# Kernel tuning notes

Measured on AMD Instinct MI355X. Metric: run time of the kernel, lower is better.

## Reference

```python
import jax, jax.numpy as jnp
import numpy as np

SPARSITY = 0.1
B, N, K = 256, 65536, 64

def setup_inputs() -> dict:
    key = jax.random.key(0)
    kx, kc = jax.random.split(key)
    x = jax.random.normal(kx, (B, N), dtype=jnp.float32)
    cluster_assignments = jax.random.randint(kc, (N,), 0, K, dtype=jnp.int32)
    cluster_weights = jnp.ones((K,), dtype=jnp.float32)
    return {"x": x, "cluster_weights": cluster_weights, "cluster_assignments": cluster_assignments}

def reference(x, cluster_weights, cluster_assignments):
    b, n = x.shape
    k = cluster_weights.shape[0]
    # cluster activation prob (context=None path): softmax(weights), same for all batch rows
    p = jax.nn.softmax(cluster_weights) * SPARSITY                      # [K]
    ku, kv = jax.random.split(jax.random.key(42))
    u = jax.random.uniform(ku, (b, n))   # drives the random permutation per (batch, cluster)
    v = jax.random.uniform(kv, (b, n))   # drives the binomial count (sum of Bernoullis)
    # Binomial(len(cluster_i), p_i) == sum of per-neuron Bernoulli(p_i) over the cluster
    bern = (v < p[cluster_assignments][None, :]).astype(jnp.int32)      # [B, N]
    counts = jax.vmap(lambda row: jax.ops.segment_sum(row, cluster_assignments, num_segments=k))(bern)  # [B, K]
    counts = jnp.maximum(counts, 1)                                     # max(1, binomial sample)
    # within-cluster uniform-random ranking: sort by (cluster, u); rank = pos - cluster_start
    sizes = jnp.bincount(cluster_assignments, length=k)                 # [K]
    starts = jnp.cumsum(sizes) - sizes                                  # exclusive cumsum [K]
    cluster_sorted = jnp.sort(cluster_assignments)                      # [N], batch-independent
    pos_in_cluster = jnp.arange(n) - starts[cluster_sorted]             # [N]
    keys = cluster_assignments.astype(jnp.float32)[None, :] + u * 0.999  # cluster-major composite key
    order = jnp.argsort(keys, axis=1)                                   # [B, N]
    mask_sorted = (pos_in_cluster[None, :] < counts[:, cluster_sorted]).astype(x.dtype)  # [B, N]
    mask = jnp.zeros_like(x).at[jnp.arange(b)[:, None], order].set(mask_sorted)
    return x * mask
```

## Files before the change

### kernel.cpp

```cpp
#include <hip/hip_runtime.h>
#include <stdint.h>

#define NROWS 256
#define NCOLS 65536
#define KCL   64
#define TMAX  20
#define NBLK  128
#define CHUNK (NCOLS / NBLK)
#define ZBLK  2048

__device__ __forceinline__ void tf2x32(uint32_t k0, uint32_t k1,
                                       uint32_t x0, uint32_t x1,
                                       uint32_t& o0, uint32_t& o1) {
  const uint32_t ks2 = k0 ^ k1 ^ 0x1BD11BDAu;
  x0 += k0; x1 += k1;
#define TFR(r) { x0 += x1; x1 = (x1 << (r)) | (x1 >> (32 - (r))); x1 ^= x0; }
  TFR(13) TFR(15) TFR(26) TFR(6)
  x0 += k1; x1 += ks2 + 1u;
  TFR(17) TFR(29) TFR(16) TFR(24)
  x0 += ks2; x1 += k0 + 2u;
  TFR(13) TFR(15) TFR(26) TFR(6)
  x0 += k0; x1 += k1 + 3u;
  TFR(17) TFR(29) TFR(16) TFR(24)
  x0 += k1; x1 += ks2 + 4u;
  TFR(13) TFR(15) TFR(26) TFR(6)
  x0 += ks2; x1 += k0 + 5u;
#undef TFR
  o0 = x0; o1 = x1;
}

__device__ __forceinline__ uint32_t jax_bits(uint32_t k0, uint32_t k1, uint32_t f) {
  uint32_t o0, o1;
  tf2x32(k0, k1, 0u, f, o0, o1);
  return o0 ^ o1;
}

__device__ __forceinline__ float bits_to_u01(uint32_t bits) {
  return __uint_as_float((bits >> 9) | 0x3f800000u) - 1.0f;
}

__device__ __forceinline__ float key_from_ubits(uint32_t ubits, float kf) {
  return __fadd_rn(kf, __fmul_rn(bits_to_u01(ubits), 0.999f));
}

__device__ __forceinline__ int wave_sum_i(int v) {
#pragma unroll
  for (int m = 1; m < 64; m <<= 1) v += __shfl_xor(v, m, 64);
  return v;
}
__device__ __forceinline__ uint32_t wave_min_u(uint32_t v) {
#pragma unroll
  for (int m = 1; m < 64; m <<= 1) {
    const uint32_t o = (uint32_t)__shfl_xor((int)v, m, 64);
    v = (o < v) ? o : v;
  }
  return v;
}
__device__ __forceinline__ int wave_min_i(int v) {
#pragma unroll
  for (int m = 1; m < 64; m <<= 1) {
    const int o = __shfl_xor(v, m, 64);
    v = (o < v) ? o : v;
  }
  return v;
}

__global__ __launch_bounds__(256)
void k_zerohist(float4* __restrict__ outv, const int* __restrict__ a,
                int* __restrict__ blockhist) {
  const int gtid = blockIdx.x * 256 + threadIdx.x;
  const float4 z = make_float4(0.f, 0.f, 0.f, 0.f);
#pragma unroll
  for (int i = 0; i < 8; ++i)
    outv[gtid + i * (ZBLK * 256)] = z;
  if (blockIdx.x < NBLK) {
    __shared__ int h[KCL];
    if (threadIdx.x < KCL) h[threadIdx.x] = 0;
    __syncthreads();
    const int base = blockIdx.x * CHUNK;
#pragma unroll
    for (int i = base + threadIdx.x; i < base + CHUNK; i += 256)
      atomicAdd(&h[a[i]], 1);
    __syncthreads();
    if (threadIdx.x < KCL) blockhist[blockIdx.x * KCL + threadIdx.x] = h[threadIdx.x];
  }
}

__global__ void k_prefix_setup(int* __restrict__ blockhist, int* __restrict__ sizes,
                               int* __restrict__ starts,
                               const float* __restrict__ w, uint32_t* __restrict__ hdr,
                               uint32_t* __restrict__ vthresh) {
  const int k = threadIdx.x;
  int acc = 0;
#pragma unroll 8
  for (int blk = 0; blk < NBLK; ++blk) {
    const int t = blockhist[blk * KCL + k];
    blockhist[blk * KCL + k] = acc;
    acc += t;
  }
  sizes[k] = acc;
  int scan = acc;
#pragma unroll
  for (int d = 1; d < 64; d <<= 1) {
    const int o = __shfl_up(scan, d, 64);
    if (k >= d) scan += o;
  }
  starts[k] = scan - acc;
  const float wk = w[k];
  float m = wk;
#pragma unroll
  for (int d = 1; d < 64; d <<= 1) m = fmaxf(m, __shfl_xor(m, d, 64));
  const float e = expf(wk - m);
  float s = e;
#pragma unroll
  for (int d = 1; d < 64; d <<= 1) s += __shfl_xor(s, d, 64);
  const float pk = (e / s) * 0.1f;
  vthresh[k] = (uint32_t)ceilf(pk * 8388608.0f);
  if (k == 0) {
    uint32_t o0, o1;
    tf2x32(0u, 42u, 0u, 0u, o0, o1); hdr[0] = o0; hdr[1] = o1;
    tf2x32(0u, 42u, 0u, 1u, o0, o1); hdr[2] = o0; hdr[3] = o1;
  }
}

__global__ __launch_bounds__(256)
void k_scatter(const int* __restrict__ a, const int* __restrict__ blockhist,
               const int* __restrict__ starts, int* __restrict__ idx_sorted) {
  __shared__ int cur[KCL];
  const int tid = threadIdx.x;
  if (tid < KCL) cur[tid] = starts[tid] + blockhist[blockIdx.x * KCL + tid];
  __syncthreads();
  const int base = blockIdx.x * CHUNK;
#pragma unroll
  for (int i = base + tid; i < base + CHUNK; i += 256) {
    const int k = a[i];
    const int slot = atomicAdd(&cur[k], 1);
    idx_sorted[slot] = i;
  }
}

__global__ __launch_bounds__(256)
void k_select(const float* __restrict__ x,
              const int* __restrict__ idx_sorted,
              const int* __restrict__ sizes,
              const int* __restrict__ starts,
              const uint32_t* __restrict__ hdr,
              const uint32_t* __restrict__ vthresh,
              float* __restrict__ out) {
  __shared__ uint32_t kbs[TMAX][256];
  const int tid = threadIdx.x;
  const int lane = tid & 63;
  const int pair = (blockIdx.x << 2) + (tid >> 6);
  const int b = pair & (NROWS - 1);
  const int k = pair >> 8;

  int sz = sizes[k];
  const int st = starts[k];
  if (sz <= 0) return;
  if (sz > TMAX * 64) sz = TMAX * 64;

  const uint32_t ku0 = hdr[0], ku1 = hdr[1], kv0 = hdr[2], kv1 = hdr[3];
  const uint32_t vt = vthresh[k];
  const float kf = (float)k;
  const uint32_t bbase = (uint32_t)(b << 16);

  int nv_next = (lane < sz) ? idx_sorted[st + lane] : 0;
  uint32_t curmin = 0xFFFFFFFFu;
  int cnt = 0;
#pragma unroll 4
  for (int t = 0; t < TMAX; ++t) {
    const int nv = nv_next;
    const int jn = lane + ((t + 1) << 6);
    nv_next = (jn < sz) ? idx_sorted[st + jn] : 0;
    const int j = lane + (t << 6);
    uint32_t kbv = 0xFFFFFFFFu;
    if (j < sz) {
      const uint32_t f = bbase + (uint32_t)nv;
      const uint32_t ubv = jax_bits(ku0, ku1, f);
      const uint32_t vbv = jax_bits(kv0, kv1, f);
      cnt += ((vbv >> 9) < vt) ? 1 : 0;
      kbv = __float_as_uint(key_from_ubits(ubv, kf));
    }
    kbs[t][tid] = kbv;
    curmin = (kbv < curmin) ? kbv : curmin;
  }
  int C = wave_sum_i(cnt);
  if (C < 1) C = 1;

  uint32_t consumed = 0;
  uint32_t Tkey;
  for (int e = 0;; ++e) {
    const uint32_t wmn = wave_min_u(curmin);
    if (e == C - 1) { Tkey = wmn; break; }
    const unsigned long long bal = __ballot(curmin == wmn);
    const int src = (int)__ffsll((long long)bal) - 1;
    if (lane == src) {
      int ct = -1;
      for (int t = 0; t < TMAX; ++t)
        if (ct < 0 && !((consumed >> t) & 1u) && kbs[t][tid] == wmn) ct = t;
      consumed |= (1u << ct);
      uint32_t nm = 0xFFFFFFFFu;
      for (int t = 0; t < TMAX; ++t) {
        const uint32_t v = ((consumed >> t) & 1u) ? 0xFFFFFFFFu : kbs[t][tid];
        nm = (v < nm) ? v : nm;
      }
      curmin = nm;
    }
  }

  int packed = 0;
#pragma unroll 4
  for (int t = 0; t < TMAX; ++t) {
    const uint32_t v = kbs[t][tid];
    packed += (v < Tkey) ? (1 << 16) : 0;
    packed += (v == Tkey) ? 1 : 0;
  }
  const int sred = wave_sum_i(packed);
  const int nbelow = sred >> 16;
  const int tieCnt = sred & 0xFFFF;
  const int r = C - nbelow;

  int cutN = 0x7FFFFFFF;
  if (r < tieCnt) {
    uint32_t cons2 = 0;
    for (int e = 0; e < r; ++e) {
      int mnN = 0x7FFFFFFF, mnT = 0;
      for (int t = 0; t < TMAX; ++t) {
        if (kbs[t][tid] == Tkey && !((cons2 >> t) & 1u)) {
          const int n = idx_sorted[st + lane + (t << 6)];
          if (n < mnN) { mnN = n; mnT = t; }
        }
      }
      const int w = wave_min_i(mnN);
      cutN = w;
      const unsigned long long bal = __ballot(mnN == w);
      const int src = (int)__ffsll((long long)bal) - 1;
      if (lane == src) cons2 |= (1u << mnT);
    }
  }

  const size_t rowoff = (size_t)b * NCOLS;
#pragma unroll 4
  for (int t = 0; t < TMAX; ++t) {
    const uint32_t v = kbs[t][tid];
    bool sel = (v < Tkey);
    if (!sel && v == Tkey) {
      if (r >= tieCnt) {
        sel = true;
      } else {
        const int n = idx_sorted[st + lane + (t << 6)];
        sel = (n <= cutN);
      }
    }
    if (sel) {
      const int n = idx_sorted[st + lane + (t << 6)];
      const size_t off = rowoff + (uint32_t)n;
      out[off] = x[off];
    }
  }
}

extern "C" void kernel_launch(void* const* d_in, const int* in_sizes, int n_in,
                              void* d_out, int out_size, void* d_ws, size_t ws_size,
                              hipStream_t stream) {
  const float* x = (const float*)d_in[0];
  const float* w = (const float*)d_in[1];
  const int* assign = (const int*)d_in[2];
  float* out = (float*)d_out;
  uint32_t* ws = (uint32_t*)d_ws;

  uint32_t* hdr       = ws;
  uint32_t* vthresh   = ws + 4;
  int*      sizes     = (int*)(ws + 68);
  int*      starts    = (int*)(ws + 132);
  int*      blockhist = (int*)(ws + 196);
  int*      idxs      = (int*)(ws + 196 + NBLK * KCL);

  k_zerohist<<<ZBLK, 256, 0, stream>>>((float4*)out, assign, blockhist);
  k_prefix_setup<<<1, 64, 0, stream>>>(blockhist, sizes, starts, w, hdr, vthresh);
  k_scatter<<<NBLK, 256, 0, stream>>>(assign, blockhist, starts, idxs);
  k_select<<<(NROWS * KCL) / 4, 256, 0, stream>>>(x, idxs, sizes, starts, hdr, vthresh, out);
  (void)n_in; (void)in_sizes; (void)ws_size;
}
```

Measured before the change: 111.2 us.

## Bound per-wave loops by cluster size, use DPP reductions, regroup blocks by cluster

The select kernel's loops now run only over the cluster's actual number of 64-wide tiles (tcap) instead of always TMAX, which skips Threefry hashing and LDS scans on padding slots. Wave reductions switch from shfl_xor loops to DPP and ds_swizzle steps, and the rotate uses a builtin. Block-to-(batch, cluster) mapping changes so each block's four waves share one cluster k, making sizes and idx_sorted reads uniform per block. A side effect is that the main loop loses its software-prefetch of indices.

```diff
diff --git a/kernel.cpp b/kernel.cpp
--- a/kernel.cpp
+++ b/kernel.cpp
@@ -14,7 +14,7 @@
                                        uint32_t& o0, uint32_t& o1) {
   const uint32_t ks2 = k0 ^ k1 ^ 0x1BD11BDAu;
   x0 += k0; x1 += k1;
-#define TFR(r) { x0 += x1; x1 = (x1 << (r)) | (x1 >> (32 - (r))); x1 ^= x0; }
+#define TFR(r) { x0 += x1; x1 = __builtin_rotateleft32(x1, (r)); x1 ^= x0; }
   TFR(13) TFR(15) TFR(26) TFR(6)
   x0 += k1; x1 += ks2 + 1u;
   TFR(17) TFR(29) TFR(16) TFR(24)
@@ -44,25 +44,26 @@
 }
 
 __device__ __forceinline__ int wave_sum_i(int v) {
-#pragma unroll
-  for (int m = 1; m < 64; m <<= 1) v += __shfl_xor(v, m, 64);
+  v += __builtin_amdgcn_update_dpp(0, v, 0xB1,  0xF, 0xF, true);
+  v += __builtin_amdgcn_update_dpp(0, v, 0x4E,  0xF, 0xF, true);
+  v += __builtin_amdgcn_update_dpp(0, v, 0x141, 0xF, 0xF, true);
+  v += __builtin_amdgcn_update_dpp(0, v, 0x140, 0xF, 0xF, true);
+  v += __builtin_amdgcn_ds_swizzle(v, 0x401F);
+  v += __shfl_xor(v, 32, 64);
   return v;
 }
 __device__ __forceinline__ uint32_t wave_min_u(uint32_t v) {
-#pragma unroll
-  for (int m = 1; m < 64; m <<= 1) {
-    const uint32_t o = (uint32_t)__shfl_xor((int)v, m, 64);
-    v = (o < v) ? o : v;
-  }
+  uint32_t o;
+  o = (uint32_t)__builtin_amdgcn_update_dpp(0, (int)v, 0xB1,  0xF, 0xF, true); v = (o < v) ? o : v;
+  o = (uint32_t)__builtin_amdgcn_update_dpp(0, (int)v, 0x4E,  0xF, 0xF, true); v = (o < v) ? o : v;
+  o = (uint32_t)__builtin_amdgcn_update_dpp(0, (int)v, 0x141, 0xF, 0xF, true); v = (o < v) ? o : v;
+  o = (uint32_t)__builtin_amdgcn_update_dpp(0, (int)v, 0x140, 0xF, 0xF, true); v = (o < v) ? o : v;
+  o = (uint32_t)__builtin_amdgcn_ds_swizzle((int)v, 0x401F);                   v = (o < v) ? o : v;
+  o = (uint32_t)__shfl_xor((int)v, 32, 64);                                    v = (o < v) ? o : v;
   return v;
 }
 __device__ __forceinline__ int wave_min_i(int v) {
-#pragma unroll
-  for (int m = 1; m < 64; m <<= 1) {
-    const int o = __shfl_xor(v, m, 64);
-    v = (o < v) ? o : v;
-  }
-  return v;
+  return (int)wave_min_u((uint32_t)v);
 }
 
 __global__ __launch_bounds__(256)
@@ -150,9 +151,9 @@
   __shared__ uint32_t kbs[TMAX][256];
   const int tid = threadIdx.x;
   const int lane = tid & 63;
-  const int pair = (blockIdx.x << 2) + (tid >> 6);
-  const int b = pair & (NROWS - 1);
-  const int k = pair >> 8;
+  const int wid = tid >> 6;
+  const int k = blockIdx.x >> 6;
+  const int b = ((blockIdx.x & 63) << 2) | wid;
 
   int sz = sizes[k];
   const int st = starts[k];
@@ -164,26 +165,37 @@
   const float kf = (float)k;
   const uint32_t bbase = (uint32_t)(b << 16);
 
-  int nv_next = (lane < sz) ? idx_sorted[st + lane] : 0;
+  const int full = sz >> 6;
+  const int rem  = sz & 63;
+  const int tcap = full + (rem ? 1 : 0);
+
   uint32_t curmin = 0xFFFFFFFFu;
   int cnt = 0;
 #pragma unroll 4
-  for (int t = 0; t < TMAX; ++t) {
-    const int nv = nv_next;
-    const int jn = lane + ((t + 1) << 6);
-    nv_next = (jn < sz) ? idx_sorted[st + jn] : 0;
-    const int j = lane + (t << 6);
+  for (int t = 0; t < full; ++t) {
+    const int nv = idx_sorted[st + lane + (t << 6)];
+    const uint32_t f = bbase + (uint32_t)nv;
+    const uint32_t ubv = jax_bits(ku0, ku1, f);
+    const uint32_t vbv = jax_bits(kv0, kv1, f);
+    cnt += ((vbv >> 9) < vt) ? 1 : 0;
+    const uint32_t kbv = __float_as_uint(key_from_ubits(ubv, kf));
+    kbs[t][tid] = kbv;
+    curmin = (kbv < curmin) ? kbv : curmin;
+  }
+  if (rem) {
     uint32_t kbv = 0xFFFFFFFFu;
-    if (j < sz) {
+    if (lane < rem) {
+      const int nv = idx_sorted[st + (full << 6) + lane];
       const uint32_t f = bbase + (uint32_t)nv;
       const uint32_t ubv = jax_bits(ku0, ku1, f);
       const uint32_t vbv = jax_bits(kv0, kv1, f);
       cnt += ((vbv >> 9) < vt) ? 1 : 0;
       kbv = __float_as_uint(key_from_ubits(ubv, kf));
     }
-    kbs[t][tid] = kbv;
+    kbs[full][tid] = kbv;
     curmin = (kbv < curmin) ? kbv : curmin;
   }
+
   int C = wave_sum_i(cnt);
   if (C < 1) C = 1;
 
@@ -196,11 +208,11 @@
     const int src = (int)__ffsll((long long)bal) - 1;
     if (lane == src) {
       int ct = -1;
-      for (int t = 0; t < TMAX; ++t)
+      for (int t = 0; t < tcap; ++t)
         if (ct < 0 && !((consumed >> t) & 1u) && kbs[t][tid] == wmn) ct = t;
       consumed |= (1u << ct);
       uint32_t nm = 0xFFFFFFFFu;
-      for (int t = 0; t < TMAX; ++t) {
+      for (int t = 0; t < tcap; ++t) {
         const uint32_t v = ((consumed >> t) & 1u) ? 0xFFFFFFFFu : kbs[t][tid];
         nm = (v < nm) ? v : nm;
       }
@@ -209,8 +221,7 @@
   }
 
   int packed = 0;
-#pragma unroll 4
-  for (int t = 0; t < TMAX; ++t) {
+  for (int t = 0; t < tcap; ++t) {
     const uint32_t v = kbs[t][tid];
     packed += (v < Tkey) ? (1 << 16) : 0;
     packed += (v == Tkey) ? 1 : 0;
@@ -225,7 +236,7 @@
     uint32_t cons2 = 0;
     for (int e = 0; e < r; ++e) {
       int mnN = 0x7FFFFFFF, mnT = 0;
-      for (int t = 0; t < TMAX; ++t) {
+      for (int t = 0; t < tcap; ++t) {
         if (kbs[t][tid] == Tkey && !((cons2 >> t) & 1u)) {
           const int n = idx_sorted[st + lane + (t << 6)];
           if (n < mnN) { mnN = n; mnT = t; }
@@ -240,12 +251,12 @@
   }
 
   const size_t rowoff = (size_t)b * NCOLS;
-#pragma unroll 4
-  for (int t = 0; t < TMAX; ++t) {
+  const bool allTies = (r >= tieCnt);
+  for (int t = 0; t < tcap; ++t) {
     const uint32_t v = kbs[t][tid];
     bool sel = (v < Tkey);
     if (!sel && v == Tkey) {
-      if (r >= tieCnt) {
+      if (allTies) {
         sel = true;
       } else {
         const int n = idx_sorted[st + lane + (t << 6)];
```

New measurement: 112.6 us. Within noise of the previous version (+1.3%).
